# Optimization experiments

Measured on AMD Instinct MI355X. Metric: run time of the kernel, lower is better.

Reference implementation:

```python
import jax, jax.numpy as jnp
import numpy as np

N = 1024   # state dimension
L = 16384  # sequence length


def setup_inputs() -> dict:
    key = jax.random.key(0)
    k_u, k_a, k_b, k_c = jax.random.split(key, 4)
    u = jax.random.normal(k_u, (L,), dtype=jnp.float32)
    # lecun_normal: std = 1/sqrt(fan_in). Shift A by -I so the discretized
    # transition matrix Ab has spectral radius < 1 (otherwise Ab^L overflows).
    A = jax.random.normal(k_a, (N, N), dtype=jnp.float32) / np.sqrt(N) - jnp.eye(N, dtype=jnp.float32)
    B = jax.random.normal(k_b, (N, 1), dtype=jnp.float32) / np.sqrt(1.0)
    C = jax.random.normal(k_c, (1, N), dtype=jnp.float32) / np.sqrt(N)
    log_step = jnp.full((1, 1), np.log(0.01), dtype=jnp.float32)
    return {"u": u, "A": A, "B": B, "C": C, "log_step": log_step}


def reference(u, A, B, C, log_step):
    # --- discretize (bilinear / Tustin transform) ---
    step = jnp.exp(log_step)[0, 0]
    I = jnp.eye(A.shape[0], dtype=A.dtype)
    BL = jnp.linalg.inv(I - (step / 2.0) * A)
    Ab = BL @ (I + (step / 2.0) * A)     # (N, N)
    Bb = (step * BL) @ B                  # (N, 1)
    Cb = C                                # (1, N)

    # --- naive_kernel: K[l] = Cb @ Ab^l @ Bb, built as a scan recurrence ---
    def body(x, _):
        k_l = (Cb @ x)[0, 0]
        return Ab @ x, k_l

    _, K = jax.lax.scan(body, Bb, None, length=u.shape[0])  # (L,)

    # --- causal convolution: y[t] = sum_{l<=t} K[l] * u[t-l] ---
    y = jnp.convolve(u, K)[: u.shape[0]]
    return y
```

## Files before the change

kernel.cpp:

```cpp
#include <hip/hip_runtime.h>
#include <hip/hip_bf16.h>
#include <math.h>

#define N_DIM 1024
#define L_SEQ 16384

typedef unsigned short ushort_t;
typedef __bf16 bf16x8 __attribute__((ext_vector_type(8)));
typedef float f32x4 __attribute__((ext_vector_type(4)));

#define FW_F32 1
#define FW_SPLIT 2
#define FW_TSPLIT 4
#define FW_ADDD 8
#define FW_MKAB 16
#define FW_TPRE 32

#define AS1 __attribute__((address_space(1)))
#define AS3 __attribute__((address_space(3)))

__device__ __forceinline__ void split2(float v, ushort_t& h, ushort_t& m) {
  union { __bf16 b; ushort_t u; } c;
  __bf16 bh = (__bf16)v;
  float fh = (float)bh;
  c.b = bh; h = c.u;
  c.b = (__bf16)(v - fh); m = c.u;
}

__global__ __launch_bounds__(256) void k_scalesplit(const float* __restrict__ A,
    const float* __restrict__ ls, float* __restrict__ E,
    ushort_t* __restrict__ set) {
  const size_t NN = (size_t)N_DIM * N_DIM;
  float hs = 0.5f * expf(ls[0]);
  int t = threadIdx.x;
  int r0 = blockIdx.x * 64 + ((t >> 4) << 2);
  int c0 = blockIdx.y * 64 + ((t & 15) << 2);
  float v[4][4];
#pragma unroll
  for (int i = 0; i < 4; ++i) {
    float4 f = *(const float4*)&A[(size_t)(r0 + i) * N_DIM + c0];
    v[i][0] = hs * f.x; v[i][1] = hs * f.y; v[i][2] = hs * f.z; v[i][3] = hs * f.w;
    *(float4*)&E[(size_t)(r0 + i) * N_DIM + c0] =
        make_float4(v[i][0], v[i][1], v[i][2], v[i][3]);
  }
  ushort_t h[4][4], m[4][4];
#pragma unroll
  for (int i = 0; i < 4; ++i)
#pragma unroll
    for (int j = 0; j < 4; ++j) split2(v[i][j], h[i][j], m[i][j]);
#pragma unroll
  for (int i = 0; i < 4; ++i) {
    size_t o = (size_t)(r0 + i) * N_DIM + c0;
    *(ushort4*)&set[o] = make_ushort4(h[i][0], h[i][1], h[i][2], h[i][3]);
    *(ushort4*)&set[NN + o] = make_ushort4(m[i][0], m[i][1], m[i][2], m[i][3]);
  }
#pragma unroll
  for (int j = 0; j < 4; ++j) {
    size_t o = (size_t)(c0 + j) * N_DIM + r0;
    *(ushort4*)&set[2 * NN + o] = make_ushort4(h[0][j], h[1][j], h[2][j], h[3][j]);
    *(ushort4*)&set[3 * NN + o] = make_ushort4(m[0][j], m[1][j], m[2][j], m[3][j]);
  }
}

__global__ __launch_bounds__(256) void k_bbinit(ushort_t* __restrict__ VTset,
    ushort_t* __restrict__ Wset, const float* __restrict__ S,
    const float* __restrict__ B, const float* __restrict__ Cm,
    const float* __restrict__ ls) {
  const size_t KR = (size_t)128 * N_DIM;
  int bx = blockIdx.x;
  if (bx >= 256) {
    int i = (bx - 256) * 256 + threadIdx.x;
    ushort_t h, m; split2(Cm[i], h, m);
    Wset[i] = h; Wset[KR + i] = m;
    return;
  }
  int row = bx * 4 + (threadIdx.x >> 6);
  int lane = threadIdx.x & 63;
  const float* Sr = S + (size_t)row * N_DIM;
  float sum = 0.f;
  for (int k = lane; k < N_DIM; k += 64) sum += Sr[k] * B[k];
  for (int off = 32; off; off >>= 1) sum += __shfl_down(sum, off);
  if (lane == 0) {
    float step = expf(ls[0]);
    float bb = step * (B[row] + sum);
    ushort_t h, m; split2(bb, h, m);
    VTset[row] = h; VTset[KR + row] = m;
  }
}

__global__ __launch_bounds__(256) void gemm4f(
    const ushort_t* __restrict__ Qa, const ushort_t* __restrict__ Qbt,
    const float* __restrict__ D, float* __restrict__ Cf,
    ushort_t* __restrict__ Oset, ushort_t* __restrict__ Oset2, int flags,
    const ushort_t* __restrict__ SkB, ushort_t* __restrict__ Ka,
    int s, int mode) {
  const size_t NN = (size_t)N_DIM * N_DIM;
  const size_t KR = (size_t)128 * N_DIM;
  __shared__ __align__(16) ushort_t lds[32768];
  int t = threadIdx.x;
  const int lane = t & 63, w = t >> 6;
  bool isSk = (mode == 2) || (mode == 1 && (int)blockIdx.y >= 16);

  if (!isSk) {
    int m0 = blockIdx.x * 64, n0 = blockIdx.y * 64;
    int r = t & 63, kc = t >> 6;
    const ushort_t* gA[2] = {Qa, Qa + NN};
    const ushort_t* gB[2] = {Qbt, Qbt + NN};
    size_t aoff = (size_t)(m0 + r) * N_DIM + kc * 8;
    size_t boff = (size_t)(n0 + r) * N_DIM + kc * 8;

    auto stage = [&](int buf, int k0) {
      ushort_t* dst = lds + buf * 8192;
#pragma unroll
      for (int L = 0; L < 2; ++L) {
        __builtin_amdgcn_global_load_lds(
            (const AS1 void*)(gA[L] + aoff + k0),
            (AS3 void*)(dst + L * 2048 + t * 8), 16, 0, 0);
        __builtin_amdgcn_global_load_lds(
            (const AS1 void*)(gB[L] + boff + k0),
            (AS3 void*)(dst + 4096 + L * 2048 + t * 8), 16, 0, 0);
      }
    };

    f32x4 acc[2][2];
#pragma unroll
    for (int i = 0; i < 2; ++i)
#pragma unroll
      for (int j = 0; j < 2; ++j) acc[i][j] = (f32x4){0.f, 0.f, 0.f, 0.f};

    const int wm = (w >> 1) * 32, wn = (w & 1) * 32;
    const int lrow = lane & 15, kg = lane >> 4;
    const int aIdx0 = kg * 512 + (wm + lrow) * 8;
    const int bIdx0 = 4096 + kg * 512 + (wn + lrow) * 8;

    stage(0, 0);
    stage(1, 32);
    stage(2, 64);
    for (int ks = 0; ks < 32; ++ks) {
      int cur = ks & 3;
      if (ks < 29) {
        stage((ks + 3) & 3, (ks + 3) * 32);
        asm volatile("s_waitcnt vmcnt(12)" ::: "memory");
      } else if (ks == 29) {
        asm volatile("s_waitcnt vmcnt(8)" ::: "memory");
      } else if (ks == 30) {
        asm volatile("s_waitcnt vmcnt(4)" ::: "memory");
      } else {
        asm volatile("s_waitcnt vmcnt(0)" ::: "memory");
      }
      __builtin_amdgcn_s_barrier();
      __builtin_amdgcn_sched_barrier(0);
      const ushort_t* buf = lds + cur * 8192;
      bf16x8 a[2][2], b[2][2];
#pragma unroll
      for (int L = 0; L < 2; ++L) {
#pragma unroll
        for (int mi = 0; mi < 2; ++mi)
          a[L][mi] = *(const bf16x8*)&buf[L * 2048 + aIdx0 + mi * 128];
#pragma unroll
        for (int ni = 0; ni < 2; ++ni)
          b[L][ni] = *(const bf16x8*)&buf[bIdx0 + L * 2048 + ni * 128];
      }
#pragma unroll
      for (int mi = 0; mi < 2; ++mi)
#pragma unroll
        for (int ni = 0; ni < 2; ++ni) {
          f32x4 c = acc[mi][ni];
          c = __builtin_amdgcn_mfma_f32_16x16x32_bf16(a[0][mi], b[0][ni], c, 0, 0, 0);
          c = __builtin_amdgcn_mfma_f32_16x16x32_bf16(a[0][mi], b[1][ni], c, 0, 0, 0);
          c = __builtin_amdgcn_mfma_f32_16x16x32_bf16(a[1][mi], b[0][ni], c, 0, 0, 0);
          c = __builtin_amdgcn_mfma_f32_16x16x32_bf16(a[1][mi], b[1][ni], c, 0, 0, 0);
          acc[mi][ni] = c;
        }
      if (ks < 31) __builtin_amdgcn_s_barrier();
    }

#pragma unroll
    for (int mi = 0; mi < 2; ++mi)
#pragma unroll
      for (int ni = 0; ni < 2; ++ni) {
        int rowb = m0 + wm + mi * 16 + kg * 4;
        int col = n0 + wn + ni * 16 + lrow;
        float vv[4];
#pragma unroll
        for (int j = 0; j < 4; ++j) vv[j] = acc[mi][ni][j];
        if (flags & FW_TPRE) {
          ushort_t h[4], m[4];
#pragma unroll
          for (int j = 0; j < 4; ++j) split2(vv[j], h[j], m[j]);
          size_t o = (size_t)col * N_DIM + rowb;
          *(ushort4*)&Oset2[2 * NN + o] = make_ushort4(h[0], h[1], h[2], h[3]);
          *(ushort4*)&Oset2[3 * NN + o] = make_ushort4(m[0], m[1], m[2], m[3]);
        }
        if (flags & FW_ADDD) {
#pragma unroll
          for (int j = 0; j < 4; ++j) vv[j] += D[(size_t)(rowb + j) * N_DIM + col];
        }
        if (flags & FW_F32) {
#pragma unroll
          for (int j = 0; j < 4; ++j) Cf[(size_t)(rowb + j) * N_DIM + col] = vv[j];
        }
        if (flags & FW_MKAB) {
#pragma unroll
          for (int j = 0; j < 4; ++j)
            vv[j] = 2.0f * vv[j] + ((rowb + j) == col ? 1.0f : 0.0f);
        }
        if (flags & (FW_SPLIT | FW_TSPLIT)) {
          ushort_t h[4], m[4];
#pragma unroll
          for (int j = 0; j < 4; ++j) split2(vv[j], h[j], m[j]);
          if (flags & FW_SPLIT) {
#pragma unroll
            for (int j = 0; j < 4; ++j) {
              size_t o = (size_t)(rowb + j) * N_DIM + col;
              Oset[o] = h[j]; Oset[NN + o] = m[j];
            }
          }
          if (flags & FW_TSPLIT) {
            size_t o = (size_t)col * N_DIM + rowb;
            *(ushort4*)&Oset[2 * NN + o] = make_ushort4(h[0], h[1], h[2], h[3]);
            *(ushort4*)&Oset[3 * NN + o] = make_ushort4(m[0], m[1], m[2], m[3]);
          }
        }
      }
    return;
  }

  int id = (mode == 1) ? ((int)blockIdx.y - 16) * 16 + (int)blockIdx.x
                       : (int)blockIdx.y * 16 + (int)blockIdx.x;
  int rt = id >> 4, ct = id & 15;
  if (rt >= ((s + 15) >> 4)) return;
  const ushort_t* Ah = Ka;
  const ushort_t* Amm = Ka + KR;
  const ushort_t* Bh = SkB;
  const ushort_t* Bm = SkB + NN;
  const int lrow = lane & 15, kg = lane >> 4;

  auto stageS = [&](int buf, int k0) {
    ushort_t* base = lds + buf * 5120;
    if (t < 128) {
      int lvl = t >> 6, rem = t & 63, kcc = rem >> 4, i = rem & 15;
      const ushort_t* src =
          (lvl ? Amm : Ah) + (size_t)(rt * 16 + i) * N_DIM + k0 + kcc * 8;
      __builtin_amdgcn_global_load_lds((const AS1 void*)src,
                                       (AS3 void*)(base + t * 8), 16, 0, 0);
    }
#pragma unroll
    for (int it2 = 0; it2 < 2; ++it2) {
      int t2 = t + it2 * 256;
      int lvl = t2 >> 8, rem = t2 & 255, kcc = rem >> 6, c = rem & 63;
      const ushort_t* src =
          (lvl ? Bm : Bh) + (size_t)(ct * 64 + c) * N_DIM + k0 + kcc * 8;
      __builtin_amdgcn_global_load_lds(
          (const AS1 void*)src, (AS3 void*)(base + 1024 + t2 * 8), 16, 0, 0);
    }
  };

  f32x4 acc = (f32x4){0.f, 0.f, 0.f, 0.f};
  const int aO = kg * 128 + lrow * 8;
  const int bO = 1024 + kg * 512 + (w * 16 + lrow) * 8;

  stageS(0, 0);
  stageS(1, 32);
  for (int ks2 = 0; ks2 < 32; ++ks2) {
    int cur = ks2 % 3;
    if (ks2 < 30) {
      stageS((ks2 + 2) % 3, (ks2 + 2) * 32);
      if (w < 2) asm volatile("s_waitcnt vmcnt(6)" ::: "memory");
      else       asm volatile("s_waitcnt vmcnt(4)" ::: "memory");
    } else if (ks2 == 30) {
      if (w < 2) asm volatile("s_waitcnt vmcnt(3)" ::: "memory");
      else       asm volatile("s_waitcnt vmcnt(2)" ::: "memory");
    } else {
      asm volatile("s_waitcnt vmcnt(0)" ::: "memory");
    }
    __builtin_amdgcn_s_barrier();
    __builtin_amdgcn_sched_barrier(0);
    const ushort_t* b = lds + cur * 5120;
    bf16x8 a0 = *(const bf16x8*)&b[aO];
    bf16x8 a1 = *(const bf16x8*)&b[aO + 512];
    bf16x8 b0v = *(const bf16x8*)&b[bO];
    bf16x8 b1v = *(const bf16x8*)&b[bO + 2048];
    acc = __builtin_amdgcn_mfma_f32_16x16x32_bf16(a0, b0v, acc, 0, 0, 0);
    acc = __builtin_amdgcn_mfma_f32_16x16x32_bf16(a0, b1v, acc, 0, 0, 0);
    acc = __builtin_amdgcn_mfma_f32_16x16x32_bf16(a1, b0v, acc, 0, 0, 0);
    acc = __builtin_amdgcn_mfma_f32_16x16x32_bf16(a1, b1v, acc, 0, 0, 0);
    if (ks2 < 31) __builtin_amdgcn_s_barrier();
  }

  int col = ct * 64 + w * 16 + lrow;
#pragma unroll
  for (int j = 0; j < 4; ++j) {
    int ir = rt * 16 + kg * 4 + j;
    if (ir < s) {
      ushort_t h, m; split2(acc[j], h, m);
      Ka[(size_t)(s + ir) * N_DIM + col] = h;
      Ka[KR + (size_t)(s + ir) * N_DIM + col] = m;
    }
  }
}

__global__ __launch_bounds__(256) void k_combine(
    const ushort_t* __restrict__ Wset, const ushort_t* __restrict__ Vset,
    float* __restrict__ Kv) {
  const size_t KR = (size_t)128 * N_DIM;
  __shared__ __align__(16) ushort_t lds[15360];
  int t = threadIdx.x;
  int rt = blockIdx.x, ct = blockIdx.y, kz = blockIdx.z;
  int kBase = kz * 256;
  const ushort_t* Ah = Wset;
  const ushort_t* Amm = Wset + KR;
  const ushort_t* Bh = Vset;
  const ushort_t* Bm = Vset + KR;
  const int lane = t & 63, w = t >> 6;
  const int lrow = lane & 15, kg = lane >> 4;

  auto stageS = [&](int buf, int k0) {
    ushort_t* base = lds + buf * 5120;
    if (t < 128) {
      int lvl = t >> 6, rem = t & 63, kcc = rem >> 4, i = rem & 15;
      const ushort_t* src =
          (lvl ? Amm : Ah) + (size_t)(rt * 16 + i) * N_DIM + k0 + kcc * 8;
      __builtin_amdgcn_global_load_lds((const AS1 void*)src,
                                       (AS3 void*)(base + t * 8), 16, 0, 0);
    }
#pragma unroll
    for (int it = 0; it < 2; ++it) {
      int t2 = t + it * 256;
      int lvl = t2 >> 8, rem = t2 & 255, kcc = rem >> 6, c = rem & 63;
      const ushort_t* src =
          (lvl ? Bm : Bh) + (size_t)(ct * 64 + c) * N_DIM + k0 + kcc * 8;
      __builtin_amdgcn_global_load_lds(
          (const AS1 void*)src, (AS3 void*)(base + 1024 + t2 * 8), 16, 0, 0);
    }
  };

  f32x4 acc = (f32x4){0.f, 0.f, 0.f, 0.f};
  const int aO = kg * 128 + lrow * 8;
  const int bO = 1024 + kg * 512 + (w * 16 + lrow) * 8;

  stageS(0, kBase);
  stageS(1, kBase + 32);
  for (int ks = 0; ks < 8; ++ks) {
    int cur = ks % 3;
    if (ks < 6) {
      stageS((ks + 2) % 3, kBase + (ks + 2) * 32);
      if (w < 2) asm volatile("s_waitcnt vmcnt(6)" ::: "memory");
      else       asm volatile("s_waitcnt vmcnt(4)" ::: "memory");
    } else if (ks == 6) {
      if (w < 2) asm volatile("s_waitcnt vmcnt(3)" ::: "memory");
      else       asm volatile("s_waitcnt vmcnt(2)" ::: "memory");
    } else {
      asm volatile("s_waitcnt vmcnt(0)" ::: "memory");
    }
    __builtin_amdgcn_s_barrier();
    __builtin_amdgcn_sched_barrier(0);
    const ushort_t* b = lds + cur * 5120;
    bf16x8 a0 = *(const bf16x8*)&b[aO];
    bf16x8 a1 = *(const bf16x8*)&b[aO + 512];
    bf16x8 b0v = *(const bf16x8*)&b[bO];
    bf16x8 b1v = *(const bf16x8*)&b[bO + 2048];
    acc = __builtin_amdgcn_mfma_f32_16x16x32_bf16(a0, b0v, acc, 0, 0, 0);
    acc = __builtin_amdgcn_mfma_f32_16x16x32_bf16(a0, b1v, acc, 0, 0, 0);
    acc = __builtin_amdgcn_mfma_f32_16x16x32_bf16(a1, b0v, acc, 0, 0, 0);
    acc = __builtin_amdgcn_mfma_f32_16x16x32_bf16(a1, b1v, acc, 0, 0, 0);
    if (ks < 7) __builtin_amdgcn_s_barrier();
  }

  int rcol = ct * 64 + w * 16 + lrow;
#pragma unroll
  for (int j = 0; j < 4; ++j) {
    int q = rt * 16 + kg * 4 + j;
    atomicAdd(&Kv[q * 128 + rcol], acc[j]);
  }
}

__global__ __launch_bounds__(256) void conv_k(const float* __restrict__ Kv,
    const float* __restrict__ u, float* __restrict__ y) {
  const int CT = 1024, CJ = 256, LCH = 1024;
  int t0 = blockIdx.x * CT;
  int l0 = blockIdx.y * LCH;
  if (l0 > t0 + CT - 1) return;
  __shared__ __align__(16) float Ks[CJ];
  __shared__ __align__(16) float us[CT + CJ + 8];
  int tid = threadIdx.x;
  float acc0 = 0.f, acc1 = 0.f, acc2 = 0.f, acc3 = 0.f;
  int ltEnd = l0 + LCH; if (ltEnd > t0 + CT) ltEnd = t0 + CT;
  for (int lt = l0; lt < ltEnd; lt += CJ) {
    __syncthreads();
    Ks[tid] = Kv[lt + tid];
    int ub = t0 - lt - (CJ - 1);
    for (int s = tid; s < CT + CJ + 4; s += 256) {
      int g = ub + s;
      us[s] = (g >= 0 && g < L_SEQ) ? u[g] : 0.f;
    }
    __syncthreads();
    const float4* u4 = (const float4*)us;
    float4 wa = u4[tid];
#pragma unroll 4
    for (int jb = 0; jb < CJ / 4; ++jb) {
      float4 wb = u4[tid + jb + 1];
      float4 k4 = *(const float4*)&Ks[CJ - 4 - (jb << 2)];
      acc0 += k4.w * wa.x + k4.z * wa.y + k4.y * wa.z + k4.x * wa.w;
      acc1 += k4.w * wa.y + k4.z * wa.z + k4.y * wa.w + k4.x * wb.x;
      acc2 += k4.w * wa.z + k4.z * wa.w + k4.y * wb.x + k4.x * wb.y;
      acc3 += k4.w * wa.w + k4.z * wb.x + k4.y * wb.y + k4.x * wb.z;
      wa = wb;
    }
  }
  int t = t0 + (tid << 2);
  atomicAdd(&y[t + 0], acc0);
  atomicAdd(&y[t + 1], acc1);
  atomicAdd(&y[t + 2], acc2);
  atomicAdd(&y[t + 3], acc3);
}


extern "C" void kernel_launch(void* const* d_in, const int* in_sizes, int n_in,
                              void* d_out, int out_size, void* d_ws, size_t ws_size,
                              hipStream_t stream) {
  const float* u  = (const float*)d_in[0];
  const float* A  = (const float*)d_in[1];
  const float* B  = (const float*)d_in[2];
  const float* Cm = (const float*)d_in[3];
  const float* ls = (const float*)d_in[4];
  float* y  = (float*)d_out;
  float* ws = (float*)d_ws;

  const int N = N_DIM;
  const size_t NN = (size_t)N * N;
  const size_t KR = (size_t)128 * N;
  float* b0 = ws;
  float* b2 = b0 + NN;
  float* Kv = b2 + NN;
  ushort_t* setA = (ushort_t*)(Kv + L_SEQ);
  ushort_t* setB = setA + 4 * NN;
  ushort_t* setC = setB + 4 * NN;
  ushort_t* VTset = setC + 4 * NN;
  ushort_t* Wset = VTset + 2 * KR;

  hipMemsetAsync(Kv, 0, (size_t)L_SEQ * sizeof(float), stream);
  hipMemsetAsync(y,  0, (size_t)L_SEQ * sizeof(float), stream);

  dim3 g16(16, 16);
  dim3 gFull(16, 20);
  dim3 gSkF(16, 4);

  k_scalesplit<<<g16, 256, 0, stream>>>(A, ls, b0, setA);
  gemm4f<<<g16, 256, 0, stream>>>(setA, setA + 2 * NN, b0, b2, setC, setB,
                                  FW_TPRE | FW_ADDD | FW_F32 | FW_SPLIT,
                                  nullptr, nullptr, 0, 0);
  gemm4f<<<g16, 256, 0, stream>>>(setC, setB + 2 * NN, b2, b0, setA, nullptr,
                                  FW_ADDD | FW_F32 | FW_MKAB | FW_SPLIT | FW_TSPLIT,
                                  nullptr, nullptr, 0, 0);
  k_bbinit<<<260, 256, 0, stream>>>(VTset, Wset, b0, B, Cm, ls);

  ushort_t* cur = setA;
  ushort_t* oth = setB;
  for (int e = 0; e < 13; ++e) {
    int right = (e < 7);
    int s = 1 << (right ? e : (e - 7));
    ushort_t* Ka = right ? VTset : Wset;
    const ushort_t* SkB = right ? cur : cur + 2 * NN;
    int fl = (e == 12) ? FW_TSPLIT : (FW_SPLIT | FW_TSPLIT);
    gemm4f<<<gFull, 256, 0, stream>>>(cur, cur + 2 * NN, nullptr, nullptr,
                                      oth, nullptr, fl, SkB, Ka, s, 1);
    ushort_t* tmp = cur; cur = oth; oth = tmp;
  }
  gemm4f<<<gSkF, 256, 0, stream>>>(cur, cur + 2 * NN, nullptr, nullptr,
                                   nullptr, nullptr, 0, cur + 2 * NN, Wset,
                                   64, 2);
  k_combine<<<dim3(8, 2, 4), 256, 0, stream>>>(Wset, VTset, Kv);
  conv_k<<<g16, 256, 0, stream>>>(Kv, u, y);
}
```

Measured before the change: 474.1 us.

## Drop final squaring GEMM; extend left Krylov block with three strip GEMMs

```diff
diff --git a/kernel.cpp b/kernel.cpp
--- a/kernel.cpp
+++ b/kernel.cpp
@@ -93,7 +93,7 @@
     const float* __restrict__ D, float* __restrict__ Cf,
     ushort_t* __restrict__ Oset, ushort_t* __restrict__ Oset2, int flags,
     const ushort_t* __restrict__ SkB, ushort_t* __restrict__ Ka,
-    int s, int mode) {
+    int srcOff, int dstOff, int cnt, int mode) {
   const size_t NN = (size_t)N_DIM * N_DIM;
   const size_t KR = (size_t)128 * N_DIM;
   __shared__ __align__(16) ushort_t lds[32768];
@@ -229,7 +229,7 @@
   int id = (mode == 1) ? ((int)blockIdx.y - 16) * 16 + (int)blockIdx.x
                        : (int)blockIdx.y * 16 + (int)blockIdx.x;
   int rt = id >> 4, ct = id & 15;
-  if (rt >= ((s + 15) >> 4)) return;
+  if (rt >= ((cnt + 15) >> 4)) return;
   const ushort_t* Ah = Ka;
   const ushort_t* Amm = Ka + KR;
   const ushort_t* Bh = SkB;
@@ -240,8 +240,8 @@
     ushort_t* base = lds + buf * 5120;
     if (t < 128) {
       int lvl = t >> 6, rem = t & 63, kcc = rem >> 4, i = rem & 15;
-      const ushort_t* src =
-          (lvl ? Amm : Ah) + (size_t)(rt * 16 + i) * N_DIM + k0 + kcc * 8;
+      const ushort_t* src = (lvl ? Amm : Ah) +
+          (size_t)(srcOff + rt * 16 + i) * N_DIM + k0 + kcc * 8;
       __builtin_amdgcn_global_load_lds((const AS1 void*)src,
                                        (AS3 void*)(base + t * 8), 16, 0, 0);
     }
@@ -292,10 +292,10 @@
 #pragma unroll
   for (int j = 0; j < 4; ++j) {
     int ir = rt * 16 + kg * 4 + j;
-    if (ir < s) {
+    if (ir < cnt) {
       ushort_t h, m; split2(acc[j], h, m);
-      Ka[(size_t)(s + ir) * N_DIM + col] = h;
-      Ka[KR + (size_t)(s + ir) * N_DIM + col] = m;
+      Ka[(size_t)(dstOff + ir) * N_DIM + col] = h;
+      Ka[KR + (size_t)(dstOff + ir) * N_DIM + col] = m;
     }
   }
 }
@@ -306,8 +306,7 @@
   const size_t KR = (size_t)128 * N_DIM;
   __shared__ __align__(16) ushort_t lds[15360];
   int t = threadIdx.x;
-  int rt = blockIdx.x, ct = blockIdx.y, kz = blockIdx.z;
-  int kBase = kz * 256;
+  int rt = blockIdx.x, ct = blockIdx.y;
   const ushort_t* Ah = Wset;
   const ushort_t* Amm = Wset + KR;
   const ushort_t* Bh = Vset;
@@ -339,15 +338,15 @@
   const int aO = kg * 128 + lrow * 8;
   const int bO = 1024 + kg * 512 + (w * 16 + lrow) * 8;
 
-  stageS(0, kBase);
-  stageS(1, kBase + 32);
-  for (int ks = 0; ks < 8; ++ks) {
+  stageS(0, 0);
+  stageS(1, 32);
+  for (int ks = 0; ks < 32; ++ks) {
     int cur = ks % 3;
-    if (ks < 6) {
-      stageS((ks + 2) % 3, kBase + (ks + 2) * 32);
+    if (ks < 30) {
+      stageS((ks + 2) % 3, (ks + 2) * 32);
       if (w < 2) asm volatile("s_waitcnt vmcnt(6)" ::: "memory");
       else       asm volatile("s_waitcnt vmcnt(4)" ::: "memory");
-    } else if (ks == 6) {
+    } else if (ks == 30) {
       if (w < 2) asm volatile("s_waitcnt vmcnt(3)" ::: "memory");
       else       asm volatile("s_waitcnt vmcnt(2)" ::: "memory");
     } else {
@@ -364,14 +363,14 @@
     acc = __builtin_amdgcn_mfma_f32_16x16x32_bf16(a0, b1v, acc, 0, 0, 0);
     acc = __builtin_amdgcn_mfma_f32_16x16x32_bf16(a1, b0v, acc, 0, 0, 0);
     acc = __builtin_amdgcn_mfma_f32_16x16x32_bf16(a1, b1v, acc, 0, 0, 0);
-    if (ks < 7) __builtin_amdgcn_s_barrier();
+    if (ks < 31) __builtin_amdgcn_s_barrier();
   }
 
   int rcol = ct * 64 + w * 16 + lrow;
 #pragma unroll
   for (int j = 0; j < 4; ++j) {
     int q = rt * 16 + kg * 4 + j;
-    atomicAdd(&Kv[q * 128 + rcol], acc[j]);
+    Kv[q * 128 + rcol] = acc[j];
   }
 }
 
@@ -439,37 +438,38 @@
   ushort_t* VTset = setC + 4 * NN;
   ushort_t* Wset = VTset + 2 * KR;
 
-  hipMemsetAsync(Kv, 0, (size_t)L_SEQ * sizeof(float), stream);
-  hipMemsetAsync(y,  0, (size_t)L_SEQ * sizeof(float), stream);
+  hipMemsetAsync(y, 0, (size_t)L_SEQ * sizeof(float), stream);
 
   dim3 g16(16, 16);
   dim3 gFull(16, 20);
-  dim3 gSkF(16, 4);
+  dim3 gSk32(16, 2);
 
   k_scalesplit<<<g16, 256, 0, stream>>>(A, ls, b0, setA);
   gemm4f<<<g16, 256, 0, stream>>>(setA, setA + 2 * NN, b0, b2, setC, setB,
                                   FW_TPRE | FW_ADDD | FW_F32 | FW_SPLIT,
-                                  nullptr, nullptr, 0, 0);
+                                  nullptr, nullptr, 0, 0, 0, 0);
   gemm4f<<<g16, 256, 0, stream>>>(setC, setB + 2 * NN, b2, b0, setA, nullptr,
                                   FW_ADDD | FW_F32 | FW_MKAB | FW_SPLIT | FW_TSPLIT,
-                                  nullptr, nullptr, 0, 0);
+                                  nullptr, nullptr, 0, 0, 0, 0);
   k_bbinit<<<260, 256, 0, stream>>>(VTset, Wset, b0, B, Cm, ls);
 
   ushort_t* cur = setA;
   ushort_t* oth = setB;
-  for (int e = 0; e < 13; ++e) {
+  for (int e = 0; e < 12; ++e) {
     int right = (e < 7);
     int s = 1 << (right ? e : (e - 7));
     ushort_t* Ka = right ? VTset : Wset;
     const ushort_t* SkB = right ? cur : cur + 2 * NN;
-    int fl = (e == 12) ? FW_TSPLIT : (FW_SPLIT | FW_TSPLIT);
+    int fl = (e == 11) ? FW_TSPLIT : (FW_SPLIT | FW_TSPLIT);
     gemm4f<<<gFull, 256, 0, stream>>>(cur, cur + 2 * NN, nullptr, nullptr,
-                                      oth, nullptr, fl, SkB, Ka, s, 1);
+                                      oth, nullptr, fl, SkB, Ka, 0, s, s, 1);
     ushort_t* tmp = cur; cur = oth; oth = tmp;
   }
-  gemm4f<<<gSkF, 256, 0, stream>>>(cur, cur + 2 * NN, nullptr, nullptr,
-                                   nullptr, nullptr, 0, cur + 2 * NN, Wset,
-                                   64, 2);
-  k_combine<<<dim3(8, 2, 4), 256, 0, stream>>>(Wset, VTset, Kv);
+  const ushort_t* Q12T = cur + 2 * NN;
+  for (int p = 0; p < 3; ++p)
+    gemm4f<<<gSk32, 256, 0, stream>>>(cur, cur, nullptr, nullptr,
+                                      nullptr, nullptr, 0, Q12T, Wset,
+                                      32 * p, 32 + 32 * p, 32, 2);
+  k_combine<<<dim3(8, 2), 256, 0, stream>>>(Wset, VTset, Kv);
   conv_k<<<g16, 256, 0, stream>>>(Kv, u, y);
 }
```

New measurement: 475.2 us. Within noise of the previous version (+0.2%).
